# Optimization experiments

Measured on AMD Instinct MI355X. Metric: run time of the kernel, lower is better.

Reference implementation:

```python
import jax, jax.numpy as jnp
import numpy as np


def setup_inputs() -> dict:
    B, C, N = 8, 512, 2048
    ks = jax.random.split(jax.random.key(0), 5)
    return {
        "src_embedding": jax.random.normal(ks[0], (B, C, N), jnp.float32),
        "tgt_embedding": jax.random.normal(ks[1], (B, C, N), jnp.float32),
        "src": jax.random.normal(ks[2], (B, 3, N), jnp.float32),
        "tgt": jax.random.normal(ks[3], (B, 3, N), jnp.float32),
        "temperature": jnp.ones((B, 1), jnp.float32),
        "gumbel_u": jax.random.uniform(ks[4], (B * N, N), jnp.float32),
    }


def reference(src_embedding, tgt_embedding, src, tgt, temperature, gumbel_u):
    B, C, N = src_embedding.shape
    # cross-attention scores: [B, N, N]
    scores = jnp.einsum('bcn,bcm->bnm', src_embedding, tgt_embedding) / jnp.sqrt(jnp.float32(C))
    scores = scores.reshape(B * N, N)
    tau = jnp.repeat(temperature.reshape(B, 1, 1), N, axis=1).reshape(-1, 1)  # [B*N, 1]
    # gumbel-softmax (hard=True, straight-through)
    u = jnp.clip(gumbel_u, 1e-6, 1.0 - 1e-6)
    g = -jnp.log(-jnp.log(u))
    y_soft = jax.nn.softmax((scores + g) / tau, axis=-1)
    idx = jnp.argmax(y_soft, axis=-1)
    y_hard = jax.nn.one_hot(idx, N, dtype=y_soft.dtype)
    scores_st = y_hard - jax.lax.stop_gradient(y_soft) + y_soft
    scores_st = scores_st.reshape(B, N, N)
    # soft correspondences: tgt @ scores^T -> [B, 3, N]
    src_corr = jnp.einsum('bcm,bnm->bcn', tgt, scores_st)
    src_mean = src.mean(axis=2, keepdims=True)
    corr_mean = src_corr.mean(axis=2, keepdims=True)
    src_c = src - src_mean
    corr_c = src_corr - corr_mean
    # 3x3 covariance per batch
    H = jnp.einsum('bcn,bdn->bcd', src_c, corr_c)
    uS, s, vh = jnp.linalg.svd(H)
    v = jnp.swapaxes(vh, -1, -2)
    uT = jnp.swapaxes(uS, -1, -2)
    r = v @ uT
    det = jax.lax.stop_gradient(jnp.linalg.det(r))  # torch code uses .item(): constant
    d = jnp.stack([jnp.ones_like(det), jnp.ones_like(det), det], axis=-1)  # [B, 3]
    R = (v * d[:, None, :]) @ uT  # v @ diag([1,1,det]) @ u^T
    t = jnp.einsum('bij,bjk->bik', -R, src_mean) + corr_mean
    return R, t.reshape(B, 3)
```

## Files before the change

### kernel.cpp

```cpp
#include <hip/hip_runtime.h>
#include <hip/hip_fp16.h>
#include <math.h>

#define NB 8
#define NC 512
#define NN 2048

typedef __attribute__((ext_vector_type(8))) _Float16 f16x8;
typedef __attribute__((ext_vector_type(4))) float f32x4;

union U8 { uint32_t u[4]; f16x8 v; };

__device__ __forceinline__ unsigned f2mono(float v) {
    unsigned b = __float_as_uint(v);
    return (b & 0x80000000u) ? ~b : (b | 0x80000000u);
}

__device__ __forceinline__ uint32_t packsplit(float a) {
    __half h = __float2half(a);
    float hf = __half2float(h);
    __half lo = __float2half(a - hf);
    return (uint32_t)__half_as_ushort(h) | ((uint32_t)__half_as_ushort(lo) << 16);
}

__device__ __forceinline__ void g2lds16(const void* g, void* l) {
    __builtin_amdgcn_global_load_lds(
        (const __attribute__((address_space(1))) void*)g,
        (__attribute__((address_space(3))) void*)l, 16, 0, 0);
}

extern "C" __global__ __launch_bounds__(256)
void prepack(const float* __restrict__ srcE, const float* __restrict__ tgtE,
             unsigned short* __restrict__ hiA, unsigned short* __restrict__ loA,
             unsigned short* __restrict__ hiB, unsigned short* __restrict__ loB)
{
    const float* in = blockIdx.y ? tgtE : srcE;
    unsigned short* hi = blockIdx.y ? hiB : hiA;
    unsigned short* lo = blockIdx.y ? loB : loA;
    const int t  = blockIdx.x;
    const int b  = t >> 7;
    const int kt = (t >> 3) & 15;
    const int nt = t & 7;
    const int k0 = kt * 32, n0 = nt * 256;

    const int tq = threadIdx.x & 63;
    const int ko = threadIdx.x >> 6;
    const int nb = n0 + tq * 4;

    const float* gin = in + (size_t)b * (NC * NN) + (size_t)(k0 + ko * 8) * NN + nb;

    float4 v[8];
#pragma unroll
    for (int j = 0; j < 8; ++j)
        v[j] = *(const float4*)(gin + (size_t)j * NN);

    const float vv[8][4] = {
        {v[0].x, v[0].y, v[0].z, v[0].w}, {v[1].x, v[1].y, v[1].z, v[1].w},
        {v[2].x, v[2].y, v[2].z, v[2].w}, {v[3].x, v[3].y, v[3].z, v[3].w},
        {v[4].x, v[4].y, v[4].z, v[4].w}, {v[5].x, v[5].y, v[5].z, v[5].w},
        {v[6].x, v[6].y, v[6].z, v[6].w}, {v[7].x, v[7].y, v[7].z, v[7].w}};

#pragma unroll
    for (int i = 0; i < 4; ++i) {
        const int n  = nb + i;
        const int s2 = (n >> 1) & 3;
        uint32_t hw[4], lw[4];
#pragma unroll
        for (int jj = 0; jj < 4; ++jj) {
            const float a0 = vv[2 * jj][i], a1 = vv[2 * jj + 1][i];
            const __half h0 = __float2half(a0);
            const __half h1 = __float2half(a1);
            const float d0 = a0 - __half2float(h0);
            const float d1 = a1 - __half2float(h1);
            hw[jj] = (uint32_t)__half_as_ushort(h0) | ((uint32_t)__half_as_ushort(h1) << 16);
            lw[jj] = (uint32_t)__half_as_ushort(__float2half(d0)) |
                     ((uint32_t)__half_as_ushort(__float2half(d1)) << 16);
        }
        const size_t rowbase = ((size_t)b * NN + n) * NC;
        const int P = kt * 4 + (ko ^ s2);
        uint4 qh, ql;
        qh.x = hw[0]; qh.y = hw[1]; qh.z = hw[2]; qh.w = hw[3];
        ql.x = lw[0]; ql.y = lw[1]; ql.z = lw[2]; ql.w = lw[3];
        *(uint4*)(hi + rowbase + (size_t)P * 8) = qh;
        *(uint4*)(lo + rowbase + (size_t)P * 8) = ql;
    }
}

extern "C" __global__ __launch_bounds__(1024)
void scores_argmax_256b(const unsigned short* __restrict__ hiA, const unsigned short* __restrict__ loA,
                        const unsigned short* __restrict__ hiB, const unsigned short* __restrict__ loB,
                        const float* __restrict__ gum,
                        unsigned long long* __restrict__ best)
{
    __shared__ unsigned short lds[2][4][8192];

    const int id = blockIdx.x;
    const int flat = (id & 7) * 64 + (id >> 3);
    const int b  = flat >> 6;
    const int nt = (flat >> 3) & 7;
    const int mt = flat & 7;
    const int n0 = nt * 256, m0 = mt * 256;

    const int tid = threadIdx.x;
    const int wv = tid >> 6;
    const int l  = tid & 63;
    const int wn = wv >> 2, wm = wv & 3;
    const int row16 = l & 15, h = l >> 4;
    const int s2 = (row16 >> 1) & 3;
    const int fo = (h ^ s2) * 8;

    const int q = wv & 3;
    const unsigned short* gp = (wn == 0) ? hiA : (wn == 1) ? loA : (wn == 2) ? hiB : loB;
    const int pan = (wn < 2) ? n0 : m0;
    const unsigned short* gl = gp + ((size_t)b * NN + pan + q * 64 + (l >> 2)) * NC + (l & 3) * 8;

#define STG(T, BUF) do {                                        \
    const unsigned short* s_ = gl + (size_t)(T) * 32;           \
    unsigned short* d_ = &lds[BUF][wn][q * 2048];               \
    g2lds16(s_,           d_);                                  \
    g2lds16(s_ + 16 * NC, d_ + 512);                            \
    g2lds16(s_ + 32 * NC, d_ + 1024);                           \
    g2lds16(s_ + 48 * NC, d_ + 1536);                           \
} while (0)

    f32x4 acc[4][4];
#pragma unroll
    for (int i = 0; i < 4; ++i)
#pragma unroll
        for (int j = 0; j < 4; ++j)
            acc[i][j] = (f32x4){0.f, 0.f, 0.f, 0.f};

    STG(0, 0);
#pragma unroll 1
    for (int t = 0; t < 16; ++t) {
        if (t < 15) {
            STG(t + 1, (t + 1) & 1);
            asm volatile("s_waitcnt vmcnt(4)" ::: "memory");
        } else {
            asm volatile("s_waitcnt vmcnt(0)" ::: "memory");
        }
        __builtin_amdgcn_sched_barrier(0);
        __builtin_amdgcn_s_barrier();
        asm volatile("" ::: "memory");

        const unsigned short (*L)[8192] = lds[t & 1];
        f16x8 bh[4], bl[4];
#pragma unroll
        for (int ms = 0; ms < 4; ++ms) {
            const int r_ = wm * 64 + ms * 16 + row16;
            bh[ms] = *(const f16x8*)&L[2][r_ * 32 + fo];
            bl[ms] = *(const f16x8*)&L[3][r_ * 32 + fo];
        }
#pragma unroll
        for (int ns = 0; ns < 4; ++ns) {
            const int r_ = wn * 64 + ns * 16 + row16;
            const f16x8 ah = *(const f16x8*)&L[0][r_ * 32 + fo];
            const f16x8 al = *(const f16x8*)&L[1][r_ * 32 + fo];
#pragma unroll
            for (int ms = 0; ms < 4; ++ms) {
                acc[ns][ms] = __builtin_amdgcn_mfma_f32_16x16x32_f16(ah, bh[ms], acc[ns][ms], 0, 0, 0);
                acc[ns][ms] = __builtin_amdgcn_mfma_f32_16x16x32_f16(al, bh[ms], acc[ns][ms], 0, 0, 0);
                acc[ns][ms] = __builtin_amdgcn_mfma_f32_16x16x32_f16(ah, bl[ms], acc[ns][ms], 0, 0, 0);
            }
        }
        asm volatile("" ::: "memory");
        __builtin_amdgcn_s_barrier();
        asm volatile("" ::: "memory");
    }
#undef STG

    const float SCL = 0.044194173824159216f;
#pragma unroll
    for (int ns = 0; ns < 4; ++ns) {
#pragma unroll
        for (int reg = 0; reg < 4; ++reg) {
            const int n = n0 + wn * 64 + ns * 16 + h * 4 + reg;
            const float* gr = gum + ((size_t)(b * NN + n)) * NN + m0 + wm * 64 + row16;
            unsigned long long bp = 0ULL;
#pragma unroll
            for (int ms = 0; ms < 4; ++ms) {
                float u = gr[ms * 16];
                u = fminf(fmaxf(u, 1e-6f), 1.0f - 1e-6f);
                const float g = -__logf(-__logf(u));
                const float val = fmaf(acc[ns][ms][reg], SCL, g);
                const int m = m0 + wm * 64 + ms * 16 + row16;
                const unsigned long long p =
                    ((unsigned long long)f2mono(val) << 32) | (unsigned)(NN - 1 - m);
                if (p > bp) bp = p;
            }
#pragma unroll
            for (int off = 8; off > 0; off >>= 1) {
                const unsigned long long o = __shfl_xor(bp, off, 16);
                if (o > bp) bp = o;
            }
            if (row16 == 0) atomicMax(&best[(size_t)b * NN + n], bp);
        }
    }
}

extern "C" __global__ __launch_bounds__(256, 2)
void scores_argmax(const float* __restrict__ srcE,
                   const float* __restrict__ tgtE,
                   const float* __restrict__ gum,
                   const float* __restrict__ temp,
                   unsigned long long* __restrict__ best)
{
    __shared__ uint32_t As[128 * 32];
    __shared__ uint32_t Bs[128 * 32];
    const int id = blockIdx.x;
    const int flat = (id & 7) * 256 + (id >> 3);
    const int mt = flat & 15;
    const int nt = (flat >> 4) & 15;
    const int b  = flat >> 8;
    const int n0 = nt * 128, m0 = mt * 128;

    const int tid = threadIdx.x;
    const int wv = tid >> 6;
    const int l  = tid & 63;
    const int wn = wv >> 1, wm = wv & 1;
    const int row16 = l & 15, h = l >> 4;

    const int snb = 4 * (tid & 31);
    const int skb = tid >> 5;
    const uint32_t sswz = (uint32_t)(tid & 7) << 2;

    const float* Ag = srcE + (size_t)b * NC * NN + n0 + snb;
    const float* Bg = tgtE + (size_t)b * NC * NN + m0 + snb;

    float4 pA[4], pB[4];
#pragma unroll
    for (int r = 0; r < 4; ++r) {
        pA[r] = *(const float4*)(Ag + (size_t)(skb + 8 * r) * NN);
        pB[r] = *(const float4*)(Bg + (size_t)(skb + 8 * r) * NN);
    }

    f32x4 acc[4][4];
#pragma unroll
    for (int i = 0; i < 4; ++i)
#pragma unroll
        for (int j = 0; j < 4; ++j)
            acc[i][j] = (f32x4){0.f, 0.f, 0.f, 0.f};

    for (int k0 = 0; k0 < NC; k0 += 32) {
        __syncthreads();
#pragma unroll
        for (int r = 0; r < 4; ++r) {
            const int k = skb + 8 * r;
            const uint32_t kx = (uint32_t)k ^ sswz;
            uint32_t* ap = &As[snb * 32 + kx];
            uint32_t* bq = &Bs[snb * 32 + kx];
            ap[0]  = packsplit(pA[r].x); ap[32] = packsplit(pA[r].y);
            ap[64] = packsplit(pA[r].z); ap[96] = packsplit(pA[r].w);
            bq[0]  = packsplit(pB[r].x); bq[32] = packsplit(pB[r].y);
            bq[64] = packsplit(pB[r].z); bq[96] = packsplit(pB[r].w);
        }
        if (k0 + 32 < NC) {
#pragma unroll
            for (int r = 0; r < 4; ++r) {
                pA[r] = *(const float4*)(Ag + (size_t)(k0 + 32 + skb + 8 * r) * NN);
                pB[r] = *(const float4*)(Bg + (size_t)(k0 + 32 + skb + 8 * r) * NN);
            }
        }
        __syncthreads();

        U8 bfh[4], bfl[4];
#pragma unroll
        for (int ms = 0; ms < 4; ++ms) {
            const int m_loc = wm * 64 + ms * 16 + row16;
            const uint32_t swz = (uint32_t)((ms * 4 + (row16 >> 2)) & 7) << 2;
            const int base = m_loc * 32;
            const uint4 r0 = *(const uint4*)&Bs[base + (((uint32_t)(h * 8 + 0)) ^ swz)];
            const uint4 r1 = *(const uint4*)&Bs[base + (((uint32_t)(h * 8 + 4)) ^ swz)];
            bfh[ms].u[0] = __builtin_amdgcn_perm(r0.y, r0.x, 0x05040100u);
            bfh[ms].u[1] = __builtin_amdgcn_perm(r0.w, r0.z, 0x05040100u);
            bfh[ms].u[2] = __builtin_amdgcn_perm(r1.y, r1.x, 0x05040100u);
            bfh[ms].u[3] = __builtin_amdgcn_perm(r1.w, r1.z, 0x05040100u);
            bfl[ms].u[0] = __builtin_amdgcn_perm(r0.y, r0.x, 0x07060302u);
            bfl[ms].u[1] = __builtin_amdgcn_perm(r0.w, r0.z, 0x07060302u);
            bfl[ms].u[2] = __builtin_amdgcn_perm(r1.y, r1.x, 0x07060302u);
            bfl[ms].u[3] = __builtin_amdgcn_perm(r1.w, r1.z, 0x07060302u);
        }

#pragma unroll
        for (int ns = 0; ns < 4; ++ns) {
            const int n_loc = wn * 64 + ns * 16 + row16;
            const uint32_t swz = (uint32_t)((ns * 4 + (row16 >> 2)) & 7) << 2;
            const int base = n_loc * 32;
            const uint4 r0 = *(const uint4*)&As[base + (((uint32_t)(h * 8 + 0)) ^ swz)];
            const uint4 r1 = *(const uint4*)&As[base + (((uint32_t)(h * 8 + 4)) ^ swz)];
            U8 ah, al;
            ah.u[0] = __builtin_amdgcn_perm(r0.y, r0.x, 0x05040100u);
            ah.u[1] = __builtin_amdgcn_perm(r0.w, r0.z, 0x05040100u);
            ah.u[2] = __builtin_amdgcn_perm(r1.y, r1.x, 0x05040100u);
            ah.u[3] = __builtin_amdgcn_perm(r1.w, r1.z, 0x05040100u);
            al.u[0] = __builtin_amdgcn_perm(r0.y, r0.x, 0x07060302u);
            al.u[1] = __builtin_amdgcn_perm(r0.w, r0.z, 0x07060302u);
            al.u[2] = __builtin_amdgcn_perm(r1.y, r1.x, 0x07060302u);
            al.u[3] = __builtin_amdgcn_perm(r1.w, r1.z, 0x07060302u);
#pragma unroll
            for (int ms = 0; ms < 4; ++ms) {
                acc[ns][ms] = __builtin_amdgcn_mfma_f32_16x16x32_f16(ah.v, bfh[ms].v, acc[ns][ms], 0, 0, 0);
                acc[ns][ms] = __builtin_amdgcn_mfma_f32_16x16x32_f16(al.v, bfh[ms].v, acc[ns][ms], 0, 0, 0);
                acc[ns][ms] = __builtin_amdgcn_mfma_f32_16x16x32_f16(ah.v, bfl[ms].v, acc[ns][ms], 0, 0, 0);
            }
        }
    }

    const float SCL = 0.044194173824159216f;
    const float tau = temp[b];
#pragma unroll
    for (int ns = 0; ns < 4; ++ns) {
#pragma unroll
        for (int reg = 0; reg < 4; ++reg) {
            const int n = n0 + wn * 64 + ns * 16 + h * 4 + reg;
            const float* gr = gum + ((size_t)(b * NN + n)) * NN + m0 + wm * 64 + row16;
            unsigned long long bp = 0ULL;
#pragma unroll
            for (int ms = 0; ms < 4; ++ms) {
                float u = gr[ms * 16];
                u = fminf(fmaxf(u, 1e-6f), 1.0f - 1e-6f);
                const float g = -logf(-logf(u));
                const float val = (acc[ns][ms][reg] * SCL + g) / tau;
                const int m = m0 + wm * 64 + ms * 16 + row16;
                const unsigned long long p =
                    ((unsigned long long)f2mono(val) << 32) | (unsigned)(NN - 1 - m);
                if (p > bp) bp = p;
            }
#pragma unroll
            for (int off = 8; off > 0; off >>= 1) {
                const unsigned long long o = __shfl_xor(bp, off, 16);
                if (o > bp) bp = o;
            }
            if (row16 == 0) atomicMax(&best[(size_t)b * NN + n], bp);
        }
    }
}

__device__ __forceinline__ double det3(const double M[3][3]) {
    return M[0][0] * (M[1][1] * M[2][2] - M[1][2] * M[2][1])
         - M[0][1] * (M[1][0] * M[2][2] - M[1][2] * M[2][0])
         + M[0][2] * (M[1][0] * M[2][1] - M[1][1] * M[2][0]);
}

extern "C" __global__ __launch_bounds__(1024)
void assemble(const float* __restrict__ src, const float* __restrict__ tgt,
              const unsigned long long* __restrict__ best, float* __restrict__ out)
{
    const int b = blockIdx.x;
    const int tid = threadIdx.x;
    float P[9] = {}, Ss[3] = {}, Sc[3] = {};
    for (int n = tid; n < NN; n += 1024) {
        const int m = (NN - 1) - (int)(unsigned)(best[(size_t)b * NN + n] & 0xffffffffu);
        float sv[3], cv[3];
#pragma unroll
        for (int c = 0; c < 3; ++c) {
            sv[c] = src[((size_t)b * 3 + c) * NN + n];
            cv[c] = tgt[((size_t)b * 3 + c) * NN + m];
            Ss[c] += sv[c];
            Sc[c] += cv[c];
        }
#pragma unroll
        for (int c = 0; c < 3; ++c)
#pragma unroll
            for (int d = 0; d < 3; ++d)
                P[c * 3 + d] = fmaf(sv[c], cv[d], P[c * 3 + d]);
    }

    float vals[15];
#pragma unroll
    for (int i = 0; i < 9; ++i) vals[i] = P[i];
#pragma unroll
    for (int i = 0; i < 3; ++i) { vals[9 + i] = Ss[i]; vals[12 + i] = Sc[i]; }

    __shared__ float red[16][15];
    const int lane = tid & 63, wv = tid >> 6;
#pragma unroll
    for (int i = 0; i < 15; ++i) {
        float v = vals[i];
        for (int off = 32; off > 0; off >>= 1) v += __shfl_down(v, off, 64);
        if (lane == 0) red[wv][i] = v;
    }
    __syncthreads();

    if (tid == 0) {
        double tot[15];
        for (int i = 0; i < 15; ++i) {
            double s = 0.0;
            for (int wq = 0; wq < 16; ++wq) s += (double)red[wq][i];
            tot[i] = s;
        }
        double smean[3], cmean[3], H[3][3];
        for (int c = 0; c < 3; ++c) { smean[c] = tot[9 + c] / NN; cmean[c] = tot[12 + c] / NN; }
        for (int c = 0; c < 3; ++c)
            for (int d = 0; d < 3; ++d)
                H[c][d] = tot[c * 3 + d] - tot[9 + c] * tot[12 + d] / NN;

        double W[3][3], V[3][3];
        for (int i = 0; i < 3; ++i)
            for (int j = 0; j < 3; ++j) { W[i][j] = H[i][j]; V[i][j] = (i == j) ? 1.0 : 0.0; }
        for (int sweep = 0; sweep < 60; ++sweep) {
            double offsum = 0.0;
            for (int p = 0; p < 2; ++p)
                for (int q = p + 1; q < 3; ++q) {
                    double al = 0, be = 0, ga = 0;
                    for (int r = 0; r < 3; ++r) {
                        al += W[r][p] * W[r][p];
                        be += W[r][q] * W[r][q];
                        ga += W[r][p] * W[r][q];
                    }
                    offsum += fabs(ga);
                    if (fabs(ga) <= 1e-15 * sqrt(al * be)) continue;
                    double zeta = (be - al) / (2.0 * ga);
                    double t = copysign(1.0, zeta) / (fabs(zeta) + sqrt(1.0 + zeta * zeta));
                    double c = 1.0 / sqrt(1.0 + t * t), s = c * t;
                    for (int r = 0; r < 3; ++r) {
                        double wp = W[r][p], wq = W[r][q];
                        W[r][p] = c * wp - s * wq;
                        W[r][q] = s * wp + c * wq;
                        double vp = V[r][p], vq = V[r][q];
                        V[r][p] = c * vp - s * vq;
                        V[r][q] = s * vp + c * vq;
                    }
                }
            if (offsum < 1e-13) break;
        }
        double S[3];
        for (int i = 0; i < 3; ++i)
            S[i] = sqrt(W[0][i] * W[0][i] + W[1][i] * W[1][i] + W[2][i] * W[2][i]);
        for (int i = 0; i < 2; ++i) {
            int mx = i;
            for (int j = i + 1; j < 3; ++j) if (S[j] > S[mx]) mx = j;
            if (mx != i) {
                double tS = S[i]; S[i] = S[mx]; S[mx] = tS;
                for (int r = 0; r < 3; ++r) {
                    double tw = W[r][i]; W[r][i] = W[r][mx]; W[r][mx] = tw;
                    double tv = V[r][i]; V[r][i] = V[r][mx]; V[r][mx] = tv;
                }
            }
        }
        double U[3][3];
        for (int i = 0; i < 3; ++i) {
            if (S[i] > 1e-12 * S[0] && S[i] > 0.0) {
                for (int r = 0; r < 3; ++r) U[r][i] = W[r][i] / S[i];
            } else {
                double ux = U[1][0] * U[2][1] - U[2][0] * U[1][1];
                double uy = U[2][0] * U[0][1] - U[0][0] * U[2][1];
                double uz = U[0][0] * U[1][1] - U[1][0] * U[0][1];
                double nr = sqrt(ux * ux + uy * uy + uz * uz);
                if (nr < 1e-30) { ux = 1.0; uy = 0.0; uz = 0.0; nr = 1.0; }
                U[0][i] = ux / nr; U[1][i] = uy / nr; U[2][i] = uz / nr;
            }
        }
        double r_[3][3];
        for (int i = 0; i < 3; ++i)
            for (int j = 0; j < 3; ++j)
                r_[i][j] = V[i][0] * U[j][0] + V[i][1] * U[j][1] + V[i][2] * U[j][2];
        double det = det3(r_);
        double R[3][3];
        for (int i = 0; i < 3; ++i)
            for (int j = 0; j < 3; ++j)
                R[i][j] = V[i][0] * U[j][0] + V[i][1] * U[j][1] + det * V[i][2] * U[j][2];
        double t_[3];
        for (int i = 0; i < 3; ++i)
            t_[i] = -(R[i][0] * smean[0] + R[i][1] * smean[1] + R[i][2] * smean[2]) + cmean[i];

        for (int i = 0; i < 3; ++i)
            for (int j = 0; j < 3; ++j)
                out[b * 9 + i * 3 + j] = (float)R[i][j];
        for (int i = 0; i < 3; ++i) out[NB * 9 + b * 3 + i] = (float)t_[i];
    }
}

extern "C" void kernel_launch(void* const* d_in, const int* in_sizes, int n_in,
                              void* d_out, int out_size, void* d_ws, size_t ws_size,
                              hipStream_t stream)
{
    const float* srcE = (const float*)d_in[0];
    const float* tgtE = (const float*)d_in[1];
    const float* src  = (const float*)d_in[2];
    const float* tgt  = (const float*)d_in[3];
    const float* temp = (const float*)d_in[4];
    const float* gum  = (const float*)d_in[5];
    float* out = (float*)d_out;
    unsigned long long* best = (unsigned long long*)d_ws;

    (void)hipMemsetAsync(best, 0, (size_t)NB * NN * sizeof(unsigned long long), stream);

    const size_t PLANE = (size_t)NB * NN * NC;
    const size_t NEED  = 131072 + 4 * PLANE * sizeof(unsigned short);
    if (ws_size >= NEED) {
        unsigned short* hiA = (unsigned short*)((char*)d_ws + 131072);
        unsigned short* loA = hiA + PLANE;
        unsigned short* hiB = loA + PLANE;
        unsigned short* loB = hiB + PLANE;
        prepack<<<dim3(1024, 2), 256, 0, stream>>>(srcE, tgtE, hiA, loA, hiB, loB);
        scores_argmax_256b<<<512, 1024, 0, stream>>>(hiA, loA, hiB, loB, gum, best);
    } else {
        scores_argmax<<<2048, 256, 0, stream>>>(srcE, tgtE, gum, temp, best);
    }
    assemble<<<NB, 1024, 0, stream>>>(src, tgt, best, out);
}
```

Measured before the change: 196.6 us.

## Re-layout packed fp16 split operands into k-tile-major panels for contiguous staging

The prepack kernel now writes the hi/lo fp16 split embeddings in a [B][k-tile][N][32] layout, with each thread handling one n column across 32 k values. Before, it used [B][N][C] rows. The scores kernel's global-to-LDS staging now reads each k-tile as a contiguous block of 64-byte rows instead of 32-element slices strided by the full row length. This is meant to improve DRAM/cache locality of the staging loads in the GEMM. The trade-off is that the prepack reads become scalar column loads rather than float4 loads.

Measured after the change: 185.7 us, median of 2. -5.6%, faster.

```diff
diff --git a/kernel.cpp b/kernel.cpp
--- a/kernel.cpp
+++ b/kernel.cpp
@@ -43,44 +43,33 @@
     const int nt = t & 7;
     const int k0 = kt * 32, n0 = nt * 256;
 
-    const int tq = threadIdx.x & 63;
-    const int ko = threadIdx.x >> 6;
-    const int nb = n0 + tq * 4;
-
-    const float* gin = in + (size_t)b * (NC * NN) + (size_t)(k0 + ko * 8) * NN + nb;
-
-    float4 v[8];
-#pragma unroll
-    for (int j = 0; j < 8; ++j)
-        v[j] = *(const float4*)(gin + (size_t)j * NN);
-
-    const float vv[8][4] = {
-        {v[0].x, v[0].y, v[0].z, v[0].w}, {v[1].x, v[1].y, v[1].z, v[1].w},
-        {v[2].x, v[2].y, v[2].z, v[2].w}, {v[3].x, v[3].y, v[3].z, v[3].w},
-        {v[4].x, v[4].y, v[4].z, v[4].w}, {v[5].x, v[5].y, v[5].z, v[5].w},
-        {v[6].x, v[6].y, v[6].z, v[6].w}, {v[7].x, v[7].y, v[7].z, v[7].w}};
-
-#pragma unroll
-    for (int i = 0; i < 4; ++i) {
-        const int n  = nb + i;
-        const int s2 = (n >> 1) & 3;
-        uint32_t hw[4], lw[4];
-#pragma unroll
-        for (int jj = 0; jj < 4; ++jj) {
-            const float a0 = vv[2 * jj][i], a1 = vv[2 * jj + 1][i];
-            const __half h0 = __float2half(a0);
-            const __half h1 = __float2half(a1);
-            const float d0 = a0 - __half2float(h0);
-            const float d1 = a1 - __half2float(h1);
-            hw[jj] = (uint32_t)__half_as_ushort(h0) | ((uint32_t)__half_as_ushort(h1) << 16);
-            lw[jj] = (uint32_t)__half_as_ushort(__float2half(d0)) |
-                     ((uint32_t)__half_as_ushort(__float2half(d1)) << 16);
-        }
-        const size_t rowbase = ((size_t)b * NN + n) * NC;
-        const int P = kt * 4 + (ko ^ s2);
+    const int n_l = threadIdx.x;
+    const int n   = n0 + n_l;
+    const int s2  = (n >> 1) & 3;
+    const float* gin = in + (size_t)b * (NC * NN) + (size_t)k0 * NN + n;
+
+    float v[32];
+#pragma unroll
+    for (int k = 0; k < 32; ++k) v[k] = gin[(size_t)k * NN];
+
+    uint32_t hw[16], lw[16];
+#pragma unroll
+    for (int j = 0; j < 16; ++j) {
+        __half h0 = __float2half(v[2*j]);
+        __half h1 = __float2half(v[2*j+1]);
+        float  d0 = v[2*j]   - __half2float(h0);
+        float  d1 = v[2*j+1] - __half2float(h1);
+        hw[j] = (uint32_t)__half_as_ushort(h0) | ((uint32_t)__half_as_ushort(h1) << 16);
+        lw[j] = (uint32_t)__half_as_ushort(__float2half(d0)) |
+                ((uint32_t)__half_as_ushort(__float2half(d1)) << 16);
+    }
+    const size_t rowbase = ((size_t)(b * 16 + kt) * NN + n) * 32;
+#pragma unroll
+    for (int o = 0; o < 4; ++o) {
+        const int P = o ^ s2;
         uint4 qh, ql;
-        qh.x = hw[0]; qh.y = hw[1]; qh.z = hw[2]; qh.w = hw[3];
-        ql.x = lw[0]; ql.y = lw[1]; ql.z = lw[2]; ql.w = lw[3];
+        qh.x = hw[4*o+0]; qh.y = hw[4*o+1]; qh.z = hw[4*o+2]; qh.w = hw[4*o+3];
+        ql.x = lw[4*o+0]; ql.y = lw[4*o+1]; ql.z = lw[4*o+2]; ql.w = lw[4*o+3];
         *(uint4*)(hi + rowbase + (size_t)P * 8) = qh;
         *(uint4*)(lo + rowbase + (size_t)P * 8) = ql;
     }
@@ -112,15 +101,15 @@
     const int q = wv & 3;
     const unsigned short* gp = (wn == 0) ? hiA : (wn == 1) ? loA : (wn == 2) ? hiB : loB;
     const int pan = (wn < 2) ? n0 : m0;
-    const unsigned short* gl = gp + ((size_t)b * NN + pan + q * 64 + (l >> 2)) * NC + (l & 3) * 8;
+    const unsigned short* gl0 = gp + ((size_t)(b * 16) * NN + pan + q * 64 + (l >> 2)) * 32 + (l & 3) * 8;
 
 #define STG(T, BUF) do {                                        \
-    const unsigned short* s_ = gl + (size_t)(T) * 32;           \
+    const unsigned short* s_ = gl0 + (size_t)(T) * (NN * 32);   \
     unsigned short* d_ = &lds[BUF][wn][q * 2048];               \
-    g2lds16(s_,           d_);                                  \
-    g2lds16(s_ + 16 * NC, d_ + 512);                            \
-    g2lds16(s_ + 32 * NC, d_ + 1024);                           \
-    g2lds16(s_ + 48 * NC, d_ + 1536);                           \
+    g2lds16(s_,            d_);                                 \
+    g2lds16(s_ + 16 * 32,  d_ + 512);                           \
+    g2lds16(s_ + 32 * 32,  d_ + 1024);                          \
+    g2lds16(s_ + 48 * 32,  d_ + 1536);                          \
 } while (0)
 
     f32x4 acc[4][4];
```
